# Performance work log

Measured on AMD Instinct MI355X. Metric: run time of the kernel, lower is better.

## Reference

```python
import jax, jax.numpy as jnp
import numpy as np

B, S, D, H = 2, 2048, 1024, 16
DK = D // H  # 64


def setup_inputs() -> dict:
    key = jax.random.key(0)
    ks = jax.random.split(key, 8)
    q = jax.random.normal(ks[0], (B, S, D), dtype=jnp.float32)
    k = jax.random.normal(ks[1], (B, S, D), dtype=jnp.float32)
    v = jax.random.normal(ks[2], (B, S, D), dtype=jnp.float32)
    mask = jax.random.randint(ks[3], (B, 1, S, S), 0, 2, dtype=jnp.int32)
    scale = 1.0 / np.sqrt(D)
    Wq = jax.random.normal(ks[4], (D, D), dtype=jnp.float32) * scale
    Wk = jax.random.normal(ks[5], (D, D), dtype=jnp.float32) * scale
    Wv = jax.random.normal(ks[6], (D, D), dtype=jnp.float32) * scale
    Wo = jax.random.normal(ks[7], (D, D), dtype=jnp.float32) * scale
    return {"q": q, "k": k, "v": v, "mask": mask,
            "Wq": Wq, "Wk": Wk, "Wv": Wv, "Wo": Wo}


def reference(q, k, v, mask, Wq, Wk, Wv, Wo):
    # Linear projections (torch nn.Linear: x @ W.T, no bias)
    qh = (q @ Wq.T).reshape(B, S, H, DK).transpose(0, 2, 1, 3)  # [B,H,S,DK]
    kh = (k @ Wk.T).reshape(B, S, H, DK).transpose(0, 2, 1, 3)
    vh = (v @ Wv.T).reshape(B, S, H, DK).transpose(0, 2, 1, 3)
    # Scaled dot-product attention with mask fill of -1e9 where mask == 0
    scores = jnp.einsum('bhqd,bhkd->bhqk', qh, kh) / jnp.sqrt(jnp.float32(DK))
    scores = jnp.where(mask == 0, jnp.float32(-1e9), scores)
    attn = jax.nn.softmax(scores, axis=-1)
    ctx = jnp.einsum('bhqk,bhkd->bhqd', attn, vh)  # [B,H,S,DK]
    ctx = ctx.transpose(0, 2, 1, 3).reshape(B, S, D)
    return ctx @ Wo.T
```

## Files before the change

kernel.cpp:

```cpp
#include <hip/hip_runtime.h>

using u16    = unsigned short;
using u32    = unsigned int;
using f32x4  = __attribute__((ext_vector_type(4))) float;
using f32x16 = __attribute__((ext_vector_type(16))) float;
using bf16x8 = __attribute__((ext_vector_type(8))) __bf16;
using u16x4  = __attribute__((ext_vector_type(4))) u16;
using u32x2  = __attribute__((ext_vector_type(2))) u32;
using u32x4  = __attribute__((ext_vector_type(4))) u32;
using i32x4  = __attribute__((ext_vector_type(4))) int;


__device__ __forceinline__ u16 f2bf(float f) {
  union { __bf16 b; u16 u; } c; c.b = (__bf16)f; return c.u;
}

typedef __attribute__((address_space(1))) const void GVoid;
typedef __attribute__((address_space(3))) void LVoid;

__device__ __forceinline__ void gload_lds16(const void* g, void* l) {
  __builtin_amdgcn_global_load_lds((GVoid*)g, (LVoid*)l, 16, 0, 0);
}

__global__ void cvt_qkv(const float* __restrict__ a, const float* __restrict__ b,
                        const float* __restrict__ c,
                        u16* __restrict__ oa, u16* __restrict__ ob, u16* __restrict__ oc) {
  int y = blockIdx.y;
  const float* s = (y == 0) ? a : (y == 1) ? b : c;
  u16* d = (y == 0) ? oa : (y == 1) ? ob : oc;
  int i = blockIdx.x * 256 + threadIdx.x;
  f32x4 v = ((const f32x4*)s)[i];
  u16x4 r;
#pragma unroll
  for (int j = 0; j < 4; ++j) r[j] = f2bf(v[j]);
  ((u16x4*)d)[i] = r;
}

__global__ void cvt_w(const float* __restrict__ a, const float* __restrict__ b,
                      const float* __restrict__ c, const float* __restrict__ dd,
                      u16* __restrict__ oa, u16* __restrict__ ob,
                      u16* __restrict__ oc, u16* __restrict__ od) {
  int y = blockIdx.y;
  const float* s = (y == 0) ? a : (y == 1) ? b : (y == 2) ? c : dd;
  u16* d = (y == 0) ? oa : (y == 1) ? ob : (y == 2) ? oc : od;
  int i = blockIdx.x * 256 + threadIdx.x;
  f32x4 v = ((const f32x4*)s)[i];
  u16x4 r;
#pragma unroll
  for (int j = 0; j < 4; ++j) r[j] = f2bf(v[j]);
  ((u16x4*)d)[i] = r;
}

__global__ void pack_mask(const int* __restrict__ m, u32* __restrict__ mp) {
  int tid = blockIdx.x * 256 + threadIdx.x;
  int q = tid & 2047, kt = (tid >> 11) & 31, b = tid >> 16;
  const i32x4* src = (const i32x4*)(m + ((size_t)(b * 2048 + q)) * 2048 + kt * 64);
  u32 w0 = 0, w1 = 0;
#pragma unroll
  for (int j = 0; j < 8; ++j) {
    i32x4 a = src[j], c = src[j + 8];
#pragma unroll
    for (int e = 0; e < 4; ++e) {
      w0 |= (a[e] != 0 ? 1u : 0u) << (j * 4 + e);
      w1 |= (c[e] != 0 ? 1u : 0u) << (j * 4 + e);
    }
  }
  ((u32x2*)mp)[((size_t)(b * 32 + kt)) * 2048 + q] = u32x2{w0, w1};
}

__global__ __launch_bounds__(256, 2) void gemm_bt(const u16* __restrict__ X,
                                                  const u16* __restrict__ W,
                                                  void* __restrict__ out, int epi) {
  __shared__ alignas(16) char lds[32768];
  const int t = threadIdx.x;
  const int lane = t & 63, wid = t >> 6;
  const int g = lane >> 4, r16 = lane & 15;
  const int wm = wid >> 1, wn = wid & 1;
  const int m0 = blockIdx.x * 128, n0 = blockIdx.y * 128;

  const u16* Xp = X;
  const u16* Wp = W;
  void* op = out;
  int e = epi;
  float qsc = 1.0f;
  if (epi < 0) {
    int z = blockIdx.z;
    Xp += (size_t)z * 4194304;
    Wp += (size_t)z * 1048576;
    op = (void*)((u16*)out + (size_t)z * 4194304);
    e = (z == 0) ? 0 : (z == 1) ? 3 : 1;
    if (z == 0) qsc = 0.18033688011f;
  }
  const char* Ab = (const char*)Xp;
  const char* Bb = (const char*)Wp;

  f32x4 acc[4][4] = {};

  for (int kk = 0; kk < 1024; kk += 64) {
#pragma unroll
    for (int i = 0; i < 4; ++i) {
      int ci = i * 256 + t;
      int row = ci >> 3;
      int cbs = ((ci & 7) << 4) ^ ((row & 7) << 4);
      gload_lds16(Ab + (size_t)(m0 + row) * 2048 + kk * 2 + cbs, lds + ci * 16);
      gload_lds16(Bb + (size_t)(n0 + row) * 2048 + kk * 2 + cbs, lds + 16384 + ci * 16);
    }
    __syncthreads();
#pragma unroll
    for (int kc = 0; kc < 2; ++kc) {
      bf16x8 af[4], bfr[4];
#pragma unroll
      for (int mf = 0; mf < 4; ++mf) {
        int row = wm * 64 + mf * 16 + r16;
        af[mf] = *(const bf16x8*)(lds + row * 128 + ((64 * kc + 16 * g) ^ ((row & 7) << 4)));
      }
#pragma unroll
      for (int nf = 0; nf < 4; ++nf) {
        int row = wn * 64 + nf * 16 + r16;
        bfr[nf] = *(const bf16x8*)(lds + 16384 + row * 128 + ((64 * kc + 16 * g) ^ ((row & 7) << 4)));
      }
#pragma unroll
      for (int mf = 0; mf < 4; ++mf)
#pragma unroll
        for (int nf = 0; nf < 4; ++nf)
          acc[mf][nf] = __builtin_amdgcn_mfma_f32_16x16x32_bf16(af[mf], bfr[nf], acc[mf][nf], 0, 0, 0);
    }
    __syncthreads();
  }

#pragma unroll
  for (int mf = 0; mf < 4; ++mf) {
#pragma unroll
    for (int nf = 0; nf < 4; ++nf) {
      int mb = m0 + wm * 64 + mf * 16 + 4 * g;
      int n = n0 + wn * 64 + nf * 16 + r16;
      if (e == 2) {
        float* O = (float*)op;
#pragma unroll
        for (int r = 0; r < 4; ++r) O[(size_t)(mb + r) * 1024 + n] = acc[mf][nf][r];
      } else if (e == 0) {
        u16* O = (u16*)op;
        int bb = mb >> 11, h = n >> 6, dk = n & 63;
#pragma unroll
        for (int r = 0; r < 4; ++r) {
          int s = (mb + r) & 2047;
          O[((size_t)(bb * 16 + h) * 2048 + s) * 64 + dk] = f2bf(acc[mf][nf][r] * qsc);
        }
      } else if (e == 3) {
        u16* O = (u16*)op;
        int h = n >> 6, dk = n & 63;
#pragma unroll
        for (int r = 0; r < 4; ++r) {
          int m = mb + r;
          int bb = m >> 11, s = m & 2047;
          size_t off16 = ((((size_t)(bb * 16 + h) * 32 + (s >> 6)) * 2 + ((s >> 5) & 1)) * 8 +
                          (dk >> 3)) * 32 + (s & 31);
          O[off16 * 8 + (dk & 7)] = f2bf(acc[mf][nf][r]);
        }
      } else {
        u16* O = (u16*)op;
        int bb = mb >> 11, s = mb & 2047, h = n >> 6, d = n & 63;
        size_t off16 = ((((size_t)(bb * 16 + h) * 32 + (s >> 6)) * 8 + ((s & 63) >> 3)) * 2 +
                        (d >> 5)) * 32 + (d & 31);
        u16x4 pv;
#pragma unroll
        for (int r = 0; r < 4; ++r) pv[r] = f2bf(acc[mf][nf][r]);
        *(u16x4*)(O + off16 * 8 + (s & 7)) = pv;
      }
    }
  }
}

struct KF { bf16x8 k0[4], k1[4]; };

__device__ __forceinline__ void loadK(KF& f, const char* p) {
#pragma unroll
  for (int c = 0; c < 4; ++c) {
    f.k0[c] = *(const bf16x8*)(p + c * 1024);
    f.k1[c] = *(const bf16x8*)(p + 4096 + c * 1024);
  }
}

__device__ __forceinline__ void attn_body(const bf16x8 (&qf)[4], KF& cur, KF& nxt,
                                          const char*& kp, const char*& vp0,
                                          const char*& vp1, const u32x2*& mptr,
                                          u32x2& mcur, int hi,
                                          f32x16& o0, f32x16& o1, float& l_run) {
  bf16x8 v0[4], v1[4];
#pragma unroll
  for (int ks = 0; ks < 4; ++ks) {
    v0[ks] = *(const bf16x8*)(vp0 + ks * 2048);
    v1[ks] = *(const bf16x8*)(vp1 + ks * 2048);
  }
  loadK(nxt, kp);
  u32x2 mnext = *mptr;
  kp += 8192; vp0 += 8192; vp1 += 8192; mptr += 2048;
  __builtin_amdgcn_sched_barrier(0);

  f32x16 s0 = {}, s1 = {};
#pragma unroll
  for (int c = 0; c < 4; ++c) {
    s0 = __builtin_amdgcn_mfma_f32_32x32x16_bf16(cur.k0[c], qf[c], s0, 0, 0, 0);
    s1 = __builtin_amdgcn_mfma_f32_32x32x16_bf16(cur.k1[c], qf[c], s1, 0, 0, 0);
  }

  u32 wa = mcur.x >> (4 * hi), wb = mcur.y >> (4 * hi);
  float ps = 0.f;
#pragma unroll
  for (int r = 0; r < 16; ++r) {
    const int bit = (r & 3) + 8 * (r >> 2);
    float p0 = __builtin_amdgcn_exp2f(s0[r]);
    float p1 = __builtin_amdgcn_exp2f(s1[r]);
    int sm0 = ((int)(wa << (31 - bit))) >> 31;
    int sm1 = ((int)(wb << (31 - bit))) >> 31;
    p0 = __uint_as_float(__float_as_uint(p0) & (u32)sm0);
    p1 = __uint_as_float(__float_as_uint(p1) & (u32)sm1);
    s0[r] = p0; s1[r] = p1;
    ps += p0 + p1;
  }
  l_run += ps;

  u32 w[16];
#pragma unroll
  for (int kb = 0; kb < 2; ++kb) {
#pragma unroll
    for (int ss = 0; ss < 2; ++ss) {
      const f32x16& sp = kb ? s1 : s0;
      u32 A0, B0, A1, B1;
      asm("v_cvt_pk_bf16_f32 %0, %1, %2" : "=v"(A0) : "v"(sp[8*ss+0]), "v"(sp[8*ss+1]));
      asm("v_cvt_pk_bf16_f32 %0, %1, %2" : "=v"(B0) : "v"(sp[8*ss+2]), "v"(sp[8*ss+3]));
      asm("v_cvt_pk_bf16_f32 %0, %1, %2" : "=v"(A1) : "v"(sp[8*ss+4]), "v"(sp[8*ss+5]));
      asm("v_cvt_pk_bf16_f32 %0, %1, %2" : "=v"(B1) : "v"(sp[8*ss+6]), "v"(sp[8*ss+7]));
      asm("v_permlane32_swap_b32 %0, %1" : "+v"(A0), "+v"(A1));
      asm("v_permlane32_swap_b32 %0, %1" : "+v"(B0), "+v"(B1));
      int f = 2 * kb + ss;
      w[4*f+0] = A0; w[4*f+1] = B0; w[4*f+2] = A1; w[4*f+3] = B1;
    }
  }

#pragma unroll
  for (int ks = 0; ks < 4; ++ks) {
    bf16x8 pa = __builtin_bit_cast(bf16x8, u32x4{w[4*ks], w[4*ks+1], w[4*ks+2], w[4*ks+3]});
    o0 = __builtin_amdgcn_mfma_f32_32x32x16_bf16(pa, v0[ks], o0, 0, 0, 0);
    o1 = __builtin_amdgcn_mfma_f32_32x32x16_bf16(pa, v1[ks], o1, 0, 0, 0);
  }
  mcur = mnext;
}

__global__ __launch_bounds__(256, 2) void attn_kern(const u16* __restrict__ Qh,
                                                    const u16* __restrict__ Kh,
                                                    const u16* __restrict__ Vt,
                                                    const u32* __restrict__ mp,
                                                    u16* __restrict__ ctx) {
  const int t = threadIdx.x;
  const int wid = t >> 6, lane = t & 63;
  const int hi = lane >> 5, l31 = lane & 31;

  const int wg = (blockIdx.x & 7) * 64 + (blockIdx.x >> 3);
  const int qt = wg & 15, bh = wg >> 4;
  const int b = bh >> 4, h = bh & 15;

  const char* qbytes = (const char*)Qh;
  const int qbase = qt * 128 + wid * 32;
  const int qg = qbase + l31;

  bf16x8 qf[4];
#pragma unroll
  for (int c = 0; c < 4; ++c)
    qf[c] = *(const bf16x8*)(qbytes + ((size_t)bh * 2048 + qg) * 128 + 32 * c + 16 * hi);

  const char* kp  = (const char*)Kh + (size_t)bh * 262144 + hi * 512 + l31 * 16;
  const char* vp0 = (const char*)Vt + (size_t)bh * 262144 + hi * 1024 + l31 * 16;
  const char* vp1 = vp0 + 512;
  const u32x2* mptr = (const u32x2*)mp + (size_t)b * 65536 + qg;

  f32x16 o0 = {}, o1 = {};
  float l_run = 0.f;

  KF A, B2;
  loadK(A, kp);
  kp += 8192;
  u32x2 mcur = *mptr;
  mptr += 2048;

#pragma unroll 1
  for (int it = 0; it < 16; ++it) {
    attn_body(qf, A, B2, kp, vp0, vp1, mptr, mcur, hi, o0, o1, l_run);
    attn_body(qf, B2, A, kp, vp0, vp1, mptr, mcur, hi, o0, o1, l_run);
  }

  l_run += __shfl_xor(l_run, 32, 64);
  float rl = 1.f / l_run;

#pragma unroll
  for (int r = 0; r < 16; ++r) {
    float rv = __shfl(rl, (r & 3) + 8 * (r >> 2) + 4 * hi, 64);
    int q = qbase + (r & 3) + 8 * (r >> 2) + 4 * hi;
    size_t rowp = ((size_t)b * 2048 + q) * 1024 + h * 64 + l31;
    ctx[rowp]      = f2bf(o0[r] * rv);
    ctx[rowp + 32] = f2bf(o1[r] * rv);
  }
}

extern "C" void kernel_launch(void* const* d_in, const int* in_sizes, int n_in,
                              void* d_out, int out_size, void* d_ws, size_t ws_size,
                              hipStream_t stream) {
  const float* q  = (const float*)d_in[0];
  const float* k  = (const float*)d_in[1];
  const float* v  = (const float*)d_in[2];
  const int* mask = (const int*)d_in[3];
  const float* Wq = (const float*)d_in[4];
  const float* Wk = (const float*)d_in[5];
  const float* Wv = (const float*)d_in[6];
  const float* Wo = (const float*)d_in[7];

  u16* ws = (u16*)d_ws;
  const size_t NX = (size_t)4096 * 1024;
  const size_t NW = (size_t)1024 * 1024;
  u16* Xq  = ws;
  u16* Wqb = ws + 3 * NX;
  u16* Qh  = Wqb + 4 * NW;
  u16* ctx = Qh + 3 * NX;
  u32* mpk = (u32*)Xq;

  cvt_qkv<<<dim3(4096, 3), 256, 0, stream>>>(q, k, v, Xq, Xq + NX, Xq + 2 * NX);
  cvt_w<<<dim3(1024, 4), 256, 0, stream>>>(Wq, Wk, Wv, Wo,
                                           Wqb, Wqb + NW, Wqb + 2 * NW, Wqb + 3 * NW);
  gemm_bt<<<dim3(32, 8, 3), 256, 0, stream>>>(Xq, Wqb, Qh, -1);
  pack_mask<<<dim3(512), 256, 0, stream>>>(mask, mpk);
  attn_kern<<<dim3(512), 256, 0, stream>>>(Qh, Qh + NX, Qh + 2 * NX, mpk, ctx);
  gemm_bt<<<dim3(32, 8, 1), 256, 0, stream>>>(ctx, Wqb + 3 * NW, d_out, 2);
}
```

Baseline: 130.7 us.

## Split attention key range across two wave groups and merge conversion kernels

The attention kernel now runs 512 threads per block, with two groups of four waves each processing half of the key sequence. Partial outputs and row sums are then combined through shared memory before normalisation. This is meant to raise wave-level parallelism and latency hiding per CU, at the cost of an LDS reduction and a tighter register budget from the new launch bounds. The three-input and four-weight fp32-to-bf16 conversion kernels are also fused into one launch, removing a launch.

```diff
diff --git a/kernel.cpp b/kernel.cpp
--- a/kernel.cpp
+++ b/kernel.cpp
@@ -22,33 +22,31 @@
   __builtin_amdgcn_global_load_lds((GVoid*)g, (LVoid*)l, 16, 0, 0);
 }
 
-__global__ void cvt_qkv(const float* __restrict__ a, const float* __restrict__ b,
-                        const float* __restrict__ c,
-                        u16* __restrict__ oa, u16* __restrict__ ob, u16* __restrict__ oc) {
-  int y = blockIdx.y;
-  const float* s = (y == 0) ? a : (y == 1) ? b : c;
-  u16* d = (y == 0) ? oa : (y == 1) ? ob : oc;
-  int i = blockIdx.x * 256 + threadIdx.x;
-  f32x4 v = ((const f32x4*)s)[i];
+__global__ void cvt_all(const float* __restrict__ q, const float* __restrict__ k,
+                        const float* __restrict__ v, const float* __restrict__ wq,
+                        const float* __restrict__ wk, const float* __restrict__ wv,
+                        const float* __restrict__ wo,
+                        u16* __restrict__ oq, u16* __restrict__ ok, u16* __restrict__ ov,
+                        u16* __restrict__ owq, u16* __restrict__ owk,
+                        u16* __restrict__ owv, u16* __restrict__ owo) {
+  size_t u = (size_t)blockIdx.x * 256 + threadIdx.x;
+  const float* s; u16* d; size_t off;
+  int sel = (int)(u >> 20);
+  if (sel < 3) {
+    s = sel == 0 ? q : sel == 1 ? k : v;
+    d = sel == 0 ? oq : sel == 1 ? ok : ov;
+    off = u & 1048575;
+  } else {
+    int wsel = (int)(u >> 18) & 3;
+    s = wsel == 0 ? wq : wsel == 1 ? wk : wsel == 2 ? wv : wo;
+    d = wsel == 0 ? owq : wsel == 1 ? owk : wsel == 2 ? owv : owo;
+    off = u & 262143;
+  }
+  f32x4 x = ((const f32x4*)s)[off];
   u16x4 r;
 #pragma unroll
-  for (int j = 0; j < 4; ++j) r[j] = f2bf(v[j]);
-  ((u16x4*)d)[i] = r;
-}
-
-__global__ void cvt_w(const float* __restrict__ a, const float* __restrict__ b,
-                      const float* __restrict__ c, const float* __restrict__ dd,
-                      u16* __restrict__ oa, u16* __restrict__ ob,
-                      u16* __restrict__ oc, u16* __restrict__ od) {
-  int y = blockIdx.y;
-  const float* s = (y == 0) ? a : (y == 1) ? b : (y == 2) ? c : dd;
-  u16* d = (y == 0) ? oa : (y == 1) ? ob : (y == 2) ? oc : od;
-  int i = blockIdx.x * 256 + threadIdx.x;
-  f32x4 v = ((const f32x4*)s)[i];
-  u16x4 r;
-#pragma unroll
-  for (int j = 0; j < 4; ++j) r[j] = f2bf(v[j]);
-  ((u16x4*)d)[i] = r;
+  for (int j = 0; j < 4; ++j) r[j] = f2bf(x[j]);
+  ((u16x4*)d)[off] = r;
 }
 
 __global__ void pack_mask(const int* __restrict__ m, u32* __restrict__ mp) {
@@ -247,13 +245,16 @@
   mcur = mnext;
 }
 
-__global__ __launch_bounds__(256, 2) void attn_kern(const u16* __restrict__ Qh,
+__global__ __launch_bounds__(512, 4) void attn_kern(const u16* __restrict__ Qh,
                                                     const u16* __restrict__ Kh,
                                                     const u16* __restrict__ Vt,
                                                     const u32* __restrict__ mp,
                                                     u16* __restrict__ ctx) {
+  __shared__ float cmb[4][32][64];
+  __shared__ float cmbl[4][64];
   const int t = threadIdx.x;
   const int wid = t >> 6, lane = t & 63;
+  const int qw = wid & 3, kh = wid >> 2;
   const int hi = lane >> 5, l31 = lane & 31;
 
   const int wg = (blockIdx.x & 7) * 64 + (blockIdx.x >> 3);
@@ -261,7 +262,7 @@
   const int b = bh >> 4, h = bh & 15;
 
   const char* qbytes = (const char*)Qh;
-  const int qbase = qt * 128 + wid * 32;
+  const int qbase = qt * 128 + qw * 32;
   const int qg = qbase + l31;
 
   bf16x8 qf[4];
@@ -269,10 +270,10 @@
   for (int c = 0; c < 4; ++c)
     qf[c] = *(const bf16x8*)(qbytes + ((size_t)bh * 2048 + qg) * 128 + 32 * c + 16 * hi);
 
-  const char* kp  = (const char*)Kh + (size_t)bh * 262144 + hi * 512 + l31 * 16;
-  const char* vp0 = (const char*)Vt + (size_t)bh * 262144 + hi * 1024 + l31 * 16;
+  const char* kp  = (const char*)Kh + (size_t)bh * 262144 + (size_t)kh * 131072 + hi * 512 + l31 * 16;
+  const char* vp0 = (const char*)Vt + (size_t)bh * 262144 + (size_t)kh * 131072 + hi * 1024 + l31 * 16;
   const char* vp1 = vp0 + 512;
-  const u32x2* mptr = (const u32x2*)mp + (size_t)b * 65536 + qg;
+  const u32x2* mptr = (const u32x2*)mp + (size_t)b * 65536 + (size_t)kh * 32768 + qg;
 
   f32x16 o0 = {}, o1 = {};
   float l_run = 0.f;
@@ -284,21 +285,39 @@
   mptr += 2048;
 
 #pragma unroll 1
-  for (int it = 0; it < 16; ++it) {
+  for (int it = 0; it < 8; ++it) {
     attn_body(qf, A, B2, kp, vp0, vp1, mptr, mcur, hi, o0, o1, l_run);
     attn_body(qf, B2, A, kp, vp0, vp1, mptr, mcur, hi, o0, o1, l_run);
   }
 
   l_run += __shfl_xor(l_run, 32, 64);
-  float rl = 1.f / l_run;
-
-#pragma unroll
-  for (int r = 0; r < 16; ++r) {
-    float rv = __shfl(rl, (r & 3) + 8 * (r >> 2) + 4 * hi, 64);
-    int q = qbase + (r & 3) + 8 * (r >> 2) + 4 * hi;
-    size_t rowp = ((size_t)b * 2048 + q) * 1024 + h * 64 + l31;
-    ctx[rowp]      = f2bf(o0[r] * rv);
-    ctx[rowp + 32] = f2bf(o1[r] * rv);
+
+  if (kh) {
+#pragma unroll
+    for (int r = 0; r < 16; ++r) {
+      cmb[qw][r][lane]      = o0[r];
+      cmb[qw][16 + r][lane] = o1[r];
+    }
+    cmbl[qw][lane] = l_run;
+  }
+  __syncthreads();
+  if (!kh) {
+#pragma unroll
+    for (int r = 0; r < 16; ++r) {
+      o0[r] += cmb[qw][r][lane];
+      o1[r] += cmb[qw][16 + r][lane];
+    }
+    l_run += cmbl[qw][lane];
+
+    float rl = 1.f / l_run;
+#pragma unroll
+    for (int r = 0; r < 16; ++r) {
+      float rv = __shfl(rl, (r & 3) + 8 * (r >> 2) + 4 * hi, 64);
+      int q = qbase + (r & 3) + 8 * (r >> 2) + 4 * hi;
+      size_t rowp = ((size_t)b * 2048 + q) * 1024 + h * 64 + l31;
+      ctx[rowp]      = f2bf(o0[r] * rv);
+      ctx[rowp + 32] = f2bf(o1[r] * rv);
+    }
   }
 }
 
@@ -323,11 +342,11 @@
   u16* ctx = Qh + 3 * NX;
   u32* mpk = (u32*)Xq;
 
-  cvt_qkv<<<dim3(4096, 3), 256, 0, stream>>>(q, k, v, Xq, Xq + NX, Xq + 2 * NX);
-  cvt_w<<<dim3(1024, 4), 256, 0, stream>>>(Wq, Wk, Wv, Wo,
+  cvt_all<<<dim3(16384), 256, 0, stream>>>(q, k, v, Wq, Wk, Wv, Wo,
+                                           Xq, Xq + NX, Xq + 2 * NX,
                                            Wqb, Wqb + NW, Wqb + 2 * NW, Wqb + 3 * NW);
   gemm_bt<<<dim3(32, 8, 3), 256, 0, stream>>>(Xq, Wqb, Qh, -1);
   pack_mask<<<dim3(512), 256, 0, stream>>>(mask, mpk);
-  attn_kern<<<dim3(512), 256, 0, stream>>>(Qh, Qh + NX, Qh + 2 * NX, mpk, ctx);
+  attn_kern<<<dim3(512), 512, 0, stream>>>(Qh, Qh + NX, Qh + 2 * NX, mpk, ctx);
   gemm_bt<<<dim3(32, 8, 1), 256, 0, stream>>>(ctx, Wqb + 3 * NW, d_out, 2);
 }
```

Result: slower. 290.5 us (+122.3%).
